# Performance work log

Hardware: AMD Instinct MI355X
Metric: run time of the kernel (lower is better)

## Reference

```python
import jax, jax.numpy as jnp
import numpy as np
import math

B, S, HID = 2, 2048, 2048
H, HKV, D, L = 16, 4, 128, 64
THETA = 10000.0
N_REP = H // HKV


def _rope(t, pos, theta=THETA):
    # t: [B, h, S, D], pos: [B, S] int
    d = t.shape[-1]
    inv_freq = 1.0 / (theta ** (jnp.arange(0, d, 2, dtype=jnp.float32) / d))  # [d/2]
    ang = pos.astype(jnp.float32)[:, :, None] * inv_freq  # [B, S, d/2]
    cos = jnp.concatenate([jnp.cos(ang), jnp.cos(ang)], axis=-1)[:, None]  # [B,1,S,d]
    sin = jnp.concatenate([jnp.sin(ang), jnp.sin(ang)], axis=-1)[:, None]
    t1, t2 = t[..., : d // 2], t[..., d // 2 :]
    rot = jnp.concatenate([-t2, t1], axis=-1)
    return t * cos + rot * sin


def setup_inputs() -> dict:
    key = jax.random.key(0)
    ks = jax.random.split(key, 9)
    sc = lambda fin: 1.0 / math.sqrt(fin)
    x = jax.random.normal(ks[0], (B, S, HID), dtype=jnp.float32)
    position_ids = jnp.broadcast_to(jnp.arange(S, dtype=jnp.int32), (B, S))
    # additive causal mask [1,1,S,S]
    causal = jnp.triu(jnp.full((S, S), -1e9, dtype=jnp.float32), k=1)
    attention_mask = causal[None, None]
    Wq = jax.random.normal(ks[1], (HID, H * D), dtype=jnp.float32) * sc(HID)
    Wk = jax.random.normal(ks[2], (HID, HKV * D), dtype=jnp.float32) * sc(HID)
    Wv = jax.random.normal(ks[3], (HID, HKV * D), dtype=jnp.float32) * sc(HID)
    Wql = jax.random.normal(ks[4], (D, L), dtype=jnp.float32) * sc(D)
    Wkl = jax.random.normal(ks[5], (D, L), dtype=jnp.float32) * sc(D)
    Wvl = jax.random.normal(ks[6], (D, L), dtype=jnp.float32) * sc(D)
    Wo = jax.random.normal(ks[7], (H * D, HID), dtype=jnp.float32) * sc(H * D)
    return {"x": x, "position_ids": position_ids, "attention_mask": attention_mask,
            "Wq": Wq, "Wk": Wk, "Wv": Wv, "Wql": Wql, "Wkl": Wkl, "Wvl": Wvl, "Wo": Wo}


def reference(x, position_ids, attention_mask, Wq, Wk, Wv, Wql, Wkl, Wvl, Wo):
    b, s, _ = x.shape
    q = (x @ Wq).reshape(b, s, H, D).transpose(0, 2, 1, 3)    # [B,H,S,D]
    k = (x @ Wk).reshape(b, s, HKV, D).transpose(0, 2, 1, 3)  # [B,HKV,S,D]
    v = (x @ Wv).reshape(b, s, HKV, D).transpose(0, 2, 1, 3)
    q = _rope(q, position_ids)
    k = _rope(k, position_ids)
    # latent compression per head-dim
    q_l = jnp.einsum('bhsd,dl->bhsl', q, Wql)  # [B,H,S,L]
    k_l = jnp.einsum('bhsd,dl->bhsl', k, Wkl)  # [B,HKV,S,L]
    v_l = jnp.einsum('bhsd,dl->bhsl', v, Wvl)
    k_l = jnp.repeat(k_l, N_REP, axis=1)  # repeat_kv -> [B,H,S,L]
    v_l = jnp.repeat(v_l, N_REP, axis=1)
    scale = math.sqrt(L)
    attn = jnp.einsum('bhql,bhkl->bhqk', q_l, k_l) / scale
    attn = attn + attention_mask
    attn = jax.nn.softmax(attn, axis=-1)
    out = jnp.einsum('bhqk,bhkl->bhql', attn, v_l)  # [B,H,S,L]
    if L < D:
        out = jnp.pad(out, ((0, 0), (0, 0), (0, 0), (0, D - L)))
    out = out.transpose(0, 2, 1, 3).reshape(b, s, H * D)
    return out @ Wo
```

## Files before the change

kernel.cpp:

```cpp
#include <hip/hip_runtime.h>
#include <cstddef>

constexpr int kB   = 2;
constexpr int kS   = 2048;
constexpr int kHID = 2048;
constexpr int kH   = 16;
constexpr int kHKV = 4;
constexpr int kD   = 128;
constexpr int kL   = 64;
constexpr int kTok = kB * kS;
constexpr int kNQKV = kH * kD + 2 * kHKV * kD;

typedef __attribute__((ext_vector_type(8))) short bf16x8;
typedef __attribute__((ext_vector_type(4))) float f32x4;

static __device__ __forceinline__ short f2bf(float f) {
  union { float f; unsigned u; } v{f};
  const unsigned r = (v.u + 0x7fff + ((v.u >> 16) & 1)) >> 16;
  return (short)r;
}
static __device__ __forceinline__ float bf2f(short s) {
  union { unsigned u; float f; } v;
  v.u = ((unsigned)(unsigned short)s) << 16;
  return v.f;
}

static __device__ __forceinline__ bf16x8 pack8(float4 a, float4 b) {
  bf16x8 r;
  r[0] = f2bf(a.x); r[1] = f2bf(a.y); r[2] = f2bf(a.z); r[3] = f2bf(a.w);
  r[4] = f2bf(b.x); r[5] = f2bf(b.y); r[6] = f2bf(b.z); r[7] = f2bf(b.w);
  return r;
}

static __device__ __forceinline__ unsigned cvt_pk_bf16(float lo, float hi) {
  unsigned r;
  asm("v_cvt_pk_bf16_f32 %0, %1, %2" : "=v"(r) : "v"(lo), "v"(hi));
  return r;
}

typedef __attribute__((address_space(3))) void       lds_void;
typedef __attribute__((address_space(1))) const void gm_void;
static __device__ __forceinline__ void gload16(const void* g, void* l) {
  __builtin_amdgcn_global_load_lds((gm_void*)g, (lds_void*)l, 16, 0, 0);
}

static __device__ __forceinline__ int2 xcd_swz(int nx, int ny) {
  int wg = blockIdx.y * nx + blockIdx.x;
  const int cpx = (nx * ny) >> 3;
  wg = (wg & 7) * cpx + (wg >> 3);
  int2 r; r.x = wg % nx; r.y = wg / nx;
  return r;
}

__global__ __launch_bounds__(256) void cvt_bf16(const float* __restrict__ in,
                                                short* __restrict__ out, int n8) {
  const int i = blockIdx.x * 256 + threadIdx.x;
  if (i >= n8) return;
  const float4 a = *(const float4*)&in[i * 8];
  const float4 b = *(const float4*)&in[i * 8 + 4];
  *(bf16x8*)&out[i * 8] = pack8(a, b);
}

__global__ __launch_bounds__(256) void trig_table(const int* __restrict__ pos,
                                                  float* __restrict__ tbl) {
  const int idx = blockIdx.x * 256 + threadIdx.x;
  if (idx >= kTok * 64) return;
  const int i = idx & 63, t = idx >> 6;
  const float p = (float)pos[t];
  const float inv_freq = expf(-(float)i * (9.210340371976184f / 64.0f));
  const float ang = p * inv_freq;
  tbl[t * 128 + i]      = cosf(ang);
  tbl[t * 128 + 64 + i] = sinf(ang);
}

template <bool REMAP>
__global__ __launch_bounds__(256) void transpose_cvt(
    const float* __restrict__ in, short* __restrict__ out,
    int Nin, int out_ld, int row_off, float scale) {
  __shared__ float T[64][65];
  const int tid = threadIdx.x;
  const int k0 = blockIdx.y * 64, n0 = blockIdx.x * 64;
  const int rr = tid >> 4;
  const int cc = tid & 15;
#pragma unroll
  for (int ii = 0; ii < 4; ++ii) {
    const int kr = rr + ii * 16;
    int gr = k0 + kr;
    if (REMAP) gr = ((gr >> 6) << 7) + (gr & 63);
    const float4 v = *(const float4*)&in[(size_t)gr * Nin + n0 + cc * 4];
    T[kr][cc * 4 + 0] = v.x * scale; T[kr][cc * 4 + 1] = v.y * scale;
    T[kr][cc * 4 + 2] = v.z * scale; T[kr][cc * 4 + 3] = v.w * scale;
  }
  __syncthreads();
#pragma unroll
  for (int ii = 0; ii < 4; ++ii) {
    const int n = rr + ii * 16;
    const short4 s4 = make_short4(f2bf(T[cc * 4 + 0][n]), f2bf(T[cc * 4 + 1][n]),
                                  f2bf(T[cc * 4 + 2][n]), f2bf(T[cc * 4 + 3][n]));
    *(short4*)&out[(size_t)(row_off + n0 + n) * out_ld + k0 + cc * 4] = s4;
  }
}

__global__ __launch_bounds__(256) void transpose_lat3(
    const float* __restrict__ Wql, const float* __restrict__ Wkl,
    const float* __restrict__ Wvl, short* __restrict__ WqlT,
    short* __restrict__ WklT, short* __restrict__ WvlT) {
  __shared__ float T[64][65];
  const float* in; short* out; float scale;
  if (blockIdx.z == 0)      { in = Wql; out = WqlT; scale = 0.125f; }
  else if (blockIdx.z == 1) { in = Wkl; out = WklT; scale = 1.0f; }
  else                      { in = Wvl; out = WvlT; scale = 1.0f; }
  const int tid = threadIdx.x;
  const int k0 = blockIdx.y * 64;
  const int rr = tid >> 4, cc = tid & 15;
#pragma unroll
  for (int ii = 0; ii < 4; ++ii) {
    const int kr = rr + ii * 16;
    const float4 v = *(const float4*)&in[(size_t)(k0 + kr) * kL + cc * 4];
    T[kr][cc * 4 + 0] = v.x * scale; T[kr][cc * 4 + 1] = v.y * scale;
    T[kr][cc * 4 + 2] = v.z * scale; T[kr][cc * 4 + 3] = v.w * scale;
  }
  __syncthreads();
#pragma unroll
  for (int ii = 0; ii < 4; ++ii) {
    const int n = rr + ii * 16;
    const short4 s4 = make_short4(f2bf(T[cc * 4 + 0][n]), f2bf(T[cc * 4 + 1][n]),
                                  f2bf(T[cc * 4 + 2][n]), f2bf(T[cc * 4 + 3][n]));
    *(short4*)&out[(size_t)n * kD + k0 + cc * 4] = s4;
  }
}

__global__ __launch_bounds__(512) void gemm_qkv8(
    const short* __restrict__ A, const short* __restrict__ Bt,
    short* __restrict__ C0, short* __restrict__ C1, short* __restrict__ C2,
    int K) {
  __shared__ short As[2][256 * 64];
  __shared__ short Bs[2][256 * 64];
  const int tid = threadIdx.x;
  const int lane = tid & 63, w = tid >> 6;
  const int lr = lane & 15, lk = lane >> 4;
  const int wm = w >> 2, wn = w & 3;
  const int2 sw = xcd_swz(kNQKV / 256, kTok / 256);
  const int row0 = sw.y * 256, col0 = sw.x * 256;
  const int NT = K >> 6;

  auto stage = [&](int kt) {
    const int b = kt & 1;
    const int k0 = kt << 6;
#pragma unroll
    for (int j = 0; j < 4; ++j) {
      const int idx = j * 512 + tid;
      const int row = idx >> 3, blk = idx & 7;
      const int gcol = k0 + ((blk ^ (row & 7)) << 3);
      gload16(A + (size_t)(row0 + row) * K + gcol, &As[b][row * 64 + blk * 8]);
    }
#pragma unroll
    for (int j = 0; j < 4; ++j) {
      const int idx = j * 512 + tid;
      const int row = idx >> 3, blk = idx & 7;
      const int gcol = k0 + ((blk ^ (row & 7)) << 3);
      gload16(Bt + (size_t)(col0 + row) * K + gcol, &Bs[b][row * 64 + blk * 8]);
    }
  };

  f32x4 acc[8][4] = {};

  stage(0);
  for (int t = 0; t < NT; ++t) {
    const int b = t & 1;
    if (t + 1 < NT) {
      stage(t + 1);
      asm volatile("s_waitcnt vmcnt(8)" ::: "memory");
    } else {
      asm volatile("s_waitcnt vmcnt(0)" ::: "memory");
    }
    __builtin_amdgcn_s_barrier();

    bf16x8 bb[4][2];
#pragma unroll
    for (int n = 0; n < 4; ++n) {
      const int row = wn * 64 + n * 16 + lr;
#pragma unroll
      for (int ch = 0; ch < 2; ++ch) {
        const int blk = (ch * 4 + lk) ^ (row & 7);
        bb[n][ch] = *(const bf16x8*)&Bs[b][row * 64 + blk * 8];
      }
    }
#pragma unroll
    for (int qm = 0; qm < 2; ++qm) {
      bf16x8 a[4][2];
#pragma unroll
      for (int j = 0; j < 4; ++j) {
        const int row = wm * 128 + (qm * 4 + j) * 16 + lr;
#pragma unroll
        for (int ch = 0; ch < 2; ++ch) {
          const int blk = (ch * 4 + lk) ^ (row & 7);
          a[j][ch] = *(const bf16x8*)&As[b][row * 64 + blk * 8];
        }
      }
      __builtin_amdgcn_s_setprio(1);
#pragma unroll
      for (int j = 0; j < 4; ++j)
#pragma unroll
        for (int n = 0; n < 4; ++n)
#pragma unroll
          for (int ch = 0; ch < 2; ++ch)
            acc[qm * 4 + j][n] = __builtin_amdgcn_mfma_f32_16x16x32_bf16(
                a[j][ch], bb[n][ch], acc[qm * 4 + j][n], 0, 0, 0);
      __builtin_amdgcn_s_setprio(0);
    }
    __builtin_amdgcn_s_barrier();
  }

  short* dst; int ld, cb;
  if (col0 < 2048)      { dst = C0; ld = 2048; cb = col0; }
  else if (col0 < 2560) { dst = C1; ld = 512;  cb = col0 - 2048; }
  else                  { dst = C2; ld = 512;  cb = col0 - 2560; }
  const int crow0 = row0 + wm * 128 + lk * 4;
  const int ccol0 = cb + wn * 64 + lr;
#pragma unroll
  for (int mf = 0; mf < 8; ++mf)
#pragma unroll
    for (int nf = 0; nf < 4; ++nf)
#pragma unroll
      for (int r = 0; r < 4; ++r)
        dst[(size_t)(crow0 + mf * 16 + r) * ld + ccol0 + nf * 16] =
            f2bf(acc[mf][nf][r]);
}

__global__ __launch_bounds__(256) void gemm_mfma(
    const short* __restrict__ A, const short* __restrict__ Bt,
    float* __restrict__ C0, int M, int N, int K) {
  __shared__ short As[128 * 32];
  __shared__ short Bs[128 * 32];
  const int tid = threadIdx.x;
  const int l = tid & 63, w = tid >> 6;
  const int lr = l & 15, lk = l >> 4;
  const int wm = w >> 1, wn = w & 1;
  const int2 sw = xcd_swz(N / 128, M / 128);
  const int row0 = sw.y * 128, col0 = sw.x * 128;

  f32x4 acc[4][4] = {};

  for (int k0 = 0; k0 < K; k0 += 32) {
    __syncthreads();
#pragma unroll
    for (int j = 0; j < 2; ++j) {
      const int idx = j * 256 + tid;
      const int r = idx >> 2, c = idx & 3;
      gload16(A  + (size_t)(row0 + r) * K + k0 + c * 8, &As[idx * 8]);
      gload16(Bt + (size_t)(col0 + r) * K + k0 + c * 8, &Bs[idx * 8]);
    }
    __syncthreads();
    bf16x8 af[4], bfr[4];
#pragma unroll
    for (int m = 0; m < 4; ++m)
      af[m] = *(const bf16x8*)&As[(wm * 64 + m * 16 + lr) * 32 + lk * 8];
#pragma unroll
    for (int n = 0; n < 4; ++n)
      bfr[n] = *(const bf16x8*)&Bs[(wn * 64 + n * 16 + lr) * 32 + lk * 8];
#pragma unroll
    for (int m = 0; m < 4; ++m)
#pragma unroll
      for (int n = 0; n < 4; ++n)
        acc[m][n] = __builtin_amdgcn_mfma_f32_16x16x32_bf16(af[m], bfr[n],
                                                            acc[m][n], 0, 0, 0);
  }

  const int crow0 = row0 + wm * 64 + lk * 4;
  const int ccol0 = col0 + wn * 64 + lr;
#pragma unroll
  for (int m = 0; m < 4; ++m)
#pragma unroll
    for (int n = 0; n < 4; ++n)
#pragma unroll
      for (int rr = 0; rr < 4; ++rr)
        C0[(size_t)(crow0 + m * 16 + rr) * N + ccol0 + n * 16] = acc[m][n][rr];
}

__global__ __launch_bounds__(256) void rope_latent_all(
    const short* __restrict__ qb, const short* __restrict__ kb,
    const short* __restrict__ vb, const short* __restrict__ WqlT,
    const short* __restrict__ WklT, const short* __restrict__ WvlT,
    const float* __restrict__ tbl, short* __restrict__ q_l,
    short* __restrict__ k_l, short* __restrict__ v_lT) {
  __shared__ short Tw[4][1280];
  const int yz = blockIdx.y;
  const short* in; const short* WT; short* out; int nh; bool ROPE, TR;
  int bh;
  if (yz < 32)      { in = qb; WT = WqlT; out = q_l;  nh = kH;   ROPE = true;  TR = false; bh = yz; }
  else if (yz < 40) { in = kb; WT = WklT; out = k_l;  nh = kHKV; ROPE = true;  TR = false; bh = yz - 32; }
  else              { in = vb; WT = WvlT; out = v_lT; nh = kHKV; ROPE = false; TR = true;  bh = yz - 40; }

  const int tid = threadIdx.x;
  const int lane = tid & 63;
  const int w = tid >> 6;
  const int lr = lane & 15;
  const int lk = lane >> 4;
  const int b = bh / nh, h = bh % nh;
  const int s0 = blockIdx.x * 64;
  const int srow = s0 + w * 16 + lr;
  const int tok = b * kS + srow;

  const short* ip = in + ((size_t)tok * nh + h) * kD + lk * 8;
  bf16x8 raw[4];
#pragma unroll
  for (int ch = 0; ch < 4; ++ch) raw[ch] = *(const bf16x8*)(ip + ch * 32);

  bf16x8 af[4];
  if (ROPE) {
    float a[4][8];
#pragma unroll
    for (int ch = 0; ch < 4; ++ch)
#pragma unroll
      for (int i = 0; i < 8; ++i) a[ch][i] = bf2f(raw[ch][i]);
    const float* tb = tbl + (size_t)tok * 128;
    float c[2][8], sn[2][8];
#pragma unroll
    for (int g = 0; g < 2; ++g) {
      const float4 cA = *(const float4*)(tb + g * 32 + lk * 8);
      const float4 cB = *(const float4*)(tb + g * 32 + lk * 8 + 4);
      const float4 sA = *(const float4*)(tb + 64 + g * 32 + lk * 8);
      const float4 sB = *(const float4*)(tb + 64 + g * 32 + lk * 8 + 4);
      c[g][0] = cA.x; c[g][1] = cA.y; c[g][2] = cA.z; c[g][3] = cA.w;
      c[g][4] = cB.x; c[g][5] = cB.y; c[g][6] = cB.z; c[g][7] = cB.w;
      sn[g][0] = sA.x; sn[g][1] = sA.y; sn[g][2] = sA.z; sn[g][3] = sA.w;
      sn[g][4] = sB.x; sn[g][5] = sB.y; sn[g][6] = sB.z; sn[g][7] = sB.w;
    }
    float o[4][8];
#pragma unroll
    for (int g = 0; g < 2; ++g)
#pragma unroll
      for (int i = 0; i < 8; ++i) {
        o[g][i]     = a[g][i]     * c[g][i] - a[g + 2][i] * sn[g][i];
        o[g + 2][i] = a[g + 2][i] * c[g][i] + a[g][i]     * sn[g][i];
      }
#pragma unroll
    for (int ch = 0; ch < 4; ++ch)
#pragma unroll
      for (int i = 0; i < 8; ++i) af[ch][i] = f2bf(o[ch][i]);
  } else {
#pragma unroll
    for (int ch = 0; ch < 4; ++ch) af[ch] = raw[ch];
  }

  f32x4 acc[4] = {};
#pragma unroll
  for (int cb = 0; cb < 4; ++cb) {
#pragma unroll
    for (int ch = 0; ch < 4; ++ch) {
      const bf16x8 bfrag =
          *(const bf16x8*)&WT[(size_t)(cb * 16 + lr) * kD + ch * 32 + lk * 8];
      acc[cb] = __builtin_amdgcn_mfma_f32_16x16x32_bf16(af[ch], bfrag,
                                                        acc[cb], 0, 0, 0);
    }
  }

  short* T = Tw[w];
  if (!TR) {
#pragma unroll
    for (int cb = 0; cb < 4; ++cb)
#pragma unroll
      for (int r = 0; r < 4; ++r)
        T[(lk * 4 + r) * 72 + cb * 16 + lr] = f2bf(acc[cb][r]);
    asm volatile("s_waitcnt lgkmcnt(0)" ::: "memory");
#pragma unroll
    for (int it = 0; it < 2; ++it) {
      const int idx = it * 64 + lane;
      const int row = idx >> 3, c8 = (idx & 7) << 3;
      *(bf16x8*)&out[((size_t)bh * kS + s0 + w * 16 + row) * kL + c8] =
          *(const bf16x8*)&T[row * 72 + c8];
    }
  } else {
#pragma unroll
    for (int cb = 0; cb < 4; ++cb)
#pragma unroll
      for (int r = 0; r < 4; ++r)
        T[(cb * 16 + lr) * 20 + lk * 4 + r] = f2bf(acc[cb][r]);
    asm volatile("s_waitcnt lgkmcnt(0)" ::: "memory");
    const size_t orow = ((size_t)bh * kL + lane) * kS + s0 + w * 16;
#pragma unroll
    for (int c = 0; c < 4; ++c)
      *(short4*)&out[orow + c * 4] = *(const short4*)&T[lane * 20 + c * 4];
  }
}

__global__ __launch_bounds__(512) void flash_attn_mfma(
    const short* __restrict__ ql, const short* __restrict__ kl,
    const short* __restrict__ vlT, short* __restrict__ attn_out) {
  constexpr int LDK = 72;
  __shared__ short Kt[2][64 * LDK];
  __shared__ short Vt[2][64 * LDK];
  __shared__ short Pt[128 * LDK];

  const int tid = threadIdx.x;
  const int lane = tid & 63;
  const int w = tid >> 6;
  const int lr = lane & 15;
  const int lk = lane >> 4;
  const int bid = blockIdx.y;
  const int bx = (bid < 8) ? (2 * bid) : (31 - 2 * bid);
  const int q0 = bx * 128;
  const int bh = blockIdx.x;
  const int b = bh >> 4, h = bh & 15;
  const int hk = h >> 2;
  const int wrow = q0 + w * 16;

  const short* qrow = ql + ((size_t)bh * kS + wrow + lr) * kL;
  bf16x8 qf[2];
  qf[0] = *(const bf16x8*)(qrow + lk * 8);
  qf[1] = *(const bf16x8*)(qrow + 32 + lk * 8);

  f32x4 Of[4] = {};
  float m_r[4], l_r[4];
#pragma unroll
  for (int r = 0; r < 4; ++r) { m_r[r] = -3.0e38f; l_r[r] = 0.f; }

  const size_t kbase = (size_t)(b * kHKV + hk) * kS * kL;
  const size_t vbase = (size_t)(b * kHKV + hk) * kL * kS;
  const int ntiles = q0 / 64 + 2;
  const int sr = tid >> 3, sc8 = (tid & 7) << 3;
  const short* kp = kl + kbase + (size_t)sr * kL + sc8;
  const short* vp = vlT + vbase + (size_t)sr * kS + sc8;

  *(bf16x8*)&Kt[0][sr * LDK + sc8] = *(const bf16x8*)kp;
  *(bf16x8*)&Vt[0][sr * LDK + sc8] = *(const bf16x8*)vp;
  __syncthreads();

  int cur = 0;
  for (int t = 0; t < ntiles; ++t) {
    const int j0 = t * 64;
    const bool pre = (t + 1 < ntiles);
    bf16x8 krn, vrn;
    if (pre) {
      krn = *(const bf16x8*)(kp + (size_t)(j0 + 64) * kL);
      vrn = *(const bf16x8*)(vp + (j0 + 64));
    }

    if (j0 <= wrow) {
      const short* Kc = &Kt[cur][0];
      const short* Vc = &Vt[cur][0];

      f32x4 Sf[4];
      __builtin_amdgcn_s_setprio(1);
#pragma unroll
      for (int cb = 0; cb < 4; ++cb) {
        f32x4 acc = {};
#pragma unroll
        for (int ch = 0; ch < 2; ++ch) {
          const bf16x8 kf = *(const bf16x8*)&Kc[(cb * 16 + lr) * LDK + ch * 32 + lk * 8];
          acc = __builtin_amdgcn_mfma_f32_16x16x32_bf16(qf[ch], kf, acc, 0, 0, 0);
        }
        Sf[cb] = acc;
      }
      __builtin_amdgcn_s_setprio(0);

      const bool diag = (j0 + 63 > wrow);
      float mt[4] = {-3.0e38f, -3.0e38f, -3.0e38f, -3.0e38f};
#pragma unroll
      for (int cb = 0; cb < 4; ++cb)
#pragma unroll
        for (int r = 0; r < 4; ++r) {
          float s = Sf[cb][r];
          if (diag && (j0 + cb * 16 + lr) > (wrow + lk * 4 + r)) s = -3.0e38f;
          Sf[cb][r] = s;
          mt[r] = fmaxf(mt[r], s);
        }
#pragma unroll
      for (int d = 1; d < 16; d <<= 1)
#pragma unroll
        for (int r = 0; r < 4; ++r) mt[r] = fmaxf(mt[r], __shfl_xor(mt[r], d));

      const bool need = (mt[0] > m_r[0] + 8.f) || (mt[1] > m_r[1] + 8.f) ||
                        (mt[2] > m_r[2] + 8.f) || (mt[3] > m_r[3] + 8.f);
      const bool resc = __any((int)need);
      float corr[4] = {1.f, 1.f, 1.f, 1.f};
      if (resc) {
#pragma unroll
        for (int r = 0; r < 4; ++r) {
          const float mnew = fmaxf(m_r[r], mt[r]);
          corr[r] = __expf(m_r[r] - mnew);
          m_r[r] = mnew;
          l_r[r] *= corr[r];
        }
      }
#pragma unroll
      for (int cb = 0; cb < 4; ++cb) {
        const float p0 = __expf(Sf[cb][0] - m_r[0]);
        const float p1 = __expf(Sf[cb][1] - m_r[1]);
        const float p2 = __expf(Sf[cb][2] - m_r[2]);
        const float p3 = __expf(Sf[cb][3] - m_r[3]);
        l_r[0] += p0; l_r[1] += p1; l_r[2] += p2; l_r[3] += p3;
        const unsigned pk01 = cvt_pk_bf16(p0, p1);
        const unsigned pk23 = cvt_pk_bf16(p2, p3);
        short* prow = &Pt[(w * 16 + lk * 4) * LDK + cb * 16 + lr];
        prow[0 * LDK] = (short)(pk01 & 0xffff);
        prow[1 * LDK] = (short)(pk01 >> 16);
        prow[2 * LDK] = (short)(pk23 & 0xffff);
        prow[3 * LDK] = (short)(pk23 >> 16);
      }
      asm volatile("s_waitcnt lgkmcnt(0)" ::: "memory");

      __builtin_amdgcn_s_setprio(1);
#pragma unroll
      for (int cb = 0; cb < 4; ++cb) {
        f32x4 acc = Of[cb];
        if (resc) {
#pragma unroll
          for (int r = 0; r < 4; ++r) acc[r] *= corr[r];
        }
#pragma unroll
        for (int ch = 0; ch < 2; ++ch) {
          const bf16x8 pf = *(const bf16x8*)&Pt[(w * 16 + lr) * LDK + ch * 32 + lk * 8];
          const bf16x8 vf = *(const bf16x8*)&Vc[(cb * 16 + lr) * LDK + ch * 32 + lk * 8];
          acc = __builtin_amdgcn_mfma_f32_16x16x32_bf16(pf, vf, acc, 0, 0, 0);
        }
        Of[cb] = acc;
      }
      __builtin_amdgcn_s_setprio(0);
    }

    if (pre) {
      *(bf16x8*)&Kt[cur ^ 1][sr * LDK + sc8] = krn;
      *(bf16x8*)&Vt[cur ^ 1][sr * LDK + sc8] = vrn;
    }
    __syncthreads();
    cur ^= 1;
  }

#pragma unroll
  for (int d = 1; d < 16; d <<= 1)
#pragma unroll
    for (int r = 0; r < 4; ++r) l_r[r] += __shfl_xor(l_r[r], d);

#pragma unroll
  for (int r = 0; r < 4; ++r) {
    const float inv = 1.f / l_r[r];
    const size_t row = (size_t)(b * kS + wrow + lk * 4 + r) * (kH * kL);
#pragma unroll
    for (int cb = 0; cb < 4; ++cb)
      attn_out[row + h * kL + cb * 16 + lr] = f2bf(Of[cb][r] * inv);
  }
}

extern "C" void kernel_launch(void* const* d_in, const int* in_sizes, int n_in,
                              void* d_out, int out_size, void* d_ws, size_t ws_size,
                              hipStream_t stream) {
  const float* x    = (const float*)d_in[0];
  const int*   pos  = (const int*)d_in[1];
  const float* Wq   = (const float*)d_in[3];
  const float* Wk   = (const float*)d_in[4];
  const float* Wv   = (const float*)d_in[5];
  const float* Wql  = (const float*)d_in[6];
  const float* Wkl  = (const float*)d_in[7];
  const float* Wvl  = (const float*)d_in[8];
  const float* Wo   = (const float*)d_in[9];
  float* out = (float*)d_out;

  char* p = (char*)d_ws;
  short* x_bf  = (short*)p; p += (size_t)kTok * kHID * 2;
  short* Wqkv  = (short*)p; p += (size_t)kNQKV * kHID * 2;
  short* WoT   = (short*)p; p += (size_t)kHID * (kH * kL) * 2;
  short* WqlT  = (short*)p; p += (size_t)kL * kD * 2;
  short* WklT  = (short*)p; p += (size_t)kL * kD * 2;
  short* WvlT  = (short*)p; p += (size_t)kL * kD * 2;
  float* tbl   = (float*)p; p += (size_t)kTok * 128 * 4;
  short* k_buf = (short*)p; p += (size_t)kTok * kHKV * kD * 2;
  short* v_buf = (short*)p; p += (size_t)kTok * kHKV * kD * 2;
  short* q_l   = (short*)p; p += (size_t)kB * kH * kS * kL * 2;
  short* k_l   = (short*)p; p += (size_t)kB * kHKV * kS * kL * 2;
  short* v_lT  = (short*)p; p += (size_t)kB * kHKV * kS * kL * 2;
  short* attn  = (short*)p;
  short* q_buf = (short*)d_out;

  cvt_bf16<<<kTok * kHID / 8 / 256, 256, 0, stream>>>(x, x_bf, kTok * kHID / 8);
  trig_table<<<kTok * 64 / 256, 256, 0, stream>>>(pos, tbl);
  transpose_cvt<false><<<dim3(kH * kD / 64, kHID / 64), 256, 0, stream>>>(
      Wq, Wqkv, kH * kD, kHID, 0, 1.0f);
  transpose_cvt<false><<<dim3(kHKV * kD / 64, kHID / 64), 256, 0, stream>>>(
      Wk, Wqkv, kHKV * kD, kHID, kH * kD, 1.0f);
  transpose_cvt<false><<<dim3(kHKV * kD / 64, kHID / 64), 256, 0, stream>>>(
      Wv, Wqkv, kHKV * kD, kHID, kH * kD + kHKV * kD, 1.0f);
  transpose_cvt<true><<<dim3(kHID / 64, (kH * kL) / 64), 256, 0, stream>>>(
      Wo, WoT, kHID, kH * kL, 0, 1.0f);
  transpose_lat3<<<dim3(1, kD / 64, 3), 256, 0, stream>>>(
      Wql, Wkl, Wvl, WqlT, WklT, WvlT);

  gemm_qkv8<<<dim3(kNQKV / 256, kTok / 256), 512, 0, stream>>>(
      x_bf, Wqkv, q_buf, k_buf, v_buf, kHID);

  rope_latent_all<<<dim3(kS / 64, 48), 256, 0, stream>>>(
      q_buf, k_buf, v_buf, WqlT, WklT, WvlT, tbl, q_l, k_l, v_lT);

  flash_attn_mfma<<<dim3(kB * kH, kS / 128), 512, 0, stream>>>(
      q_l, k_l, v_lT, attn);

  gemm_mfma<<<dim3(kHID / 128, kTok / 128), 256, 0, stream>>>(
      attn, WoT, out, kTok, kHID, kH * kL);
}
```

Before: 211.7 us.

## Merge QKV weight transposes, rewrite output GEMM with double-buffered swizzled tiles

The three Wq/Wk/Wv transpose-convert launches become one kernel that picks its source matrix per block. The output projection GEMM is rewritten with 256x128 tiles, 512 threads, K-step 64, double-buffered XOR-swizzled LDS, and async prefetch overlapped with MFMA via vmcnt waits. The flash attention mask loop now skips the per-element causal check on off-diagonal tiles. The aim is to cut launch overhead, LDS bank conflicts and load stalls in the output GEMM. The cost is higher LDS and register use per block, which may lower occupancy.

```diff
diff --git a/kernel.cpp b/kernel.cpp
--- a/kernel.cpp
+++ b/kernel.cpp
@@ -71,6 +71,34 @@
   const float ang = p * inv_freq;
   tbl[t * 128 + i]      = cosf(ang);
   tbl[t * 128 + 64 + i] = sinf(ang);
+}
+
+__global__ __launch_bounds__(256) void transpose_qkv(
+    const float* __restrict__ Wq, const float* __restrict__ Wk,
+    const float* __restrict__ Wv, short* __restrict__ out) {
+  __shared__ float T[64][65];
+  const int n0 = blockIdx.x * 64, k0 = blockIdx.y * 64;
+  const float* in; int Nin, nl0;
+  if (n0 < 2048)      { in = Wq; Nin = 2048; nl0 = n0; }
+  else if (n0 < 2560) { in = Wk; Nin = 512;  nl0 = n0 - 2048; }
+  else                { in = Wv; Nin = 512;  nl0 = n0 - 2560; }
+  const int tid = threadIdx.x;
+  const int rr = tid >> 4, cc = tid & 15;
+#pragma unroll
+  for (int ii = 0; ii < 4; ++ii) {
+    const int kr = rr + ii * 16;
+    const float4 v = *(const float4*)&in[(size_t)(k0 + kr) * Nin + nl0 + cc * 4];
+    T[kr][cc * 4 + 0] = v.x; T[kr][cc * 4 + 1] = v.y;
+    T[kr][cc * 4 + 2] = v.z; T[kr][cc * 4 + 3] = v.w;
+  }
+  __syncthreads();
+#pragma unroll
+  for (int ii = 0; ii < 4; ++ii) {
+    const int n = rr + ii * 16;
+    const short4 s4 = make_short4(f2bf(T[cc * 4 + 0][n]), f2bf(T[cc * 4 + 1][n]),
+                                  f2bf(T[cc * 4 + 2][n]), f2bf(T[cc * 4 + 3][n]));
+    *(short4*)&out[(size_t)(n0 + n) * kHID + k0 + cc * 4] = s4;
+  }
 }
 
 template <bool REMAP>
@@ -228,54 +256,96 @@
             f2bf(acc[mf][nf][r]);
 }
 
-__global__ __launch_bounds__(256) void gemm_mfma(
+__global__ __launch_bounds__(512) void gemm_out8(
     const short* __restrict__ A, const short* __restrict__ Bt,
-    float* __restrict__ C0, int M, int N, int K) {
-  __shared__ short As[128 * 32];
-  __shared__ short Bs[128 * 32];
+    float* __restrict__ C, int M, int N, int K) {
+  __shared__ short As[2][256 * 64];
+  __shared__ short Bs[2][128 * 64];
   const int tid = threadIdx.x;
-  const int l = tid & 63, w = tid >> 6;
-  const int lr = l & 15, lk = l >> 4;
-  const int wm = w >> 1, wn = w & 1;
-  const int2 sw = xcd_swz(N / 128, M / 128);
-  const int row0 = sw.y * 128, col0 = sw.x * 128;
-
-  f32x4 acc[4][4] = {};
-
-  for (int k0 = 0; k0 < K; k0 += 32) {
-    __syncthreads();
+  const int lane = tid & 63, w = tid >> 6;
+  const int lr = lane & 15, lk = lane >> 4;
+  const int wm = w >> 2, wn = w & 3;
+  const int2 sw = xcd_swz(N / 128, M / 256);
+  const int row0 = sw.y * 256, col0 = sw.x * 128;
+  const int NT = K >> 6;
+
+  auto stage = [&](int kt) {
+    const int b = kt & 1;
+    const int k0 = kt << 6;
+#pragma unroll
+    for (int j = 0; j < 4; ++j) {
+      const int idx = j * 512 + tid;
+      const int row = idx >> 3, blk = idx & 7;
+      const int gcol = k0 + ((blk ^ (row & 7)) << 3);
+      gload16(A + (size_t)(row0 + row) * K + gcol, &As[b][row * 64 + blk * 8]);
+    }
 #pragma unroll
     for (int j = 0; j < 2; ++j) {
-      const int idx = j * 256 + tid;
-      const int r = idx >> 2, c = idx & 3;
-      gload16(A  + (size_t)(row0 + r) * K + k0 + c * 8, &As[idx * 8]);
-      gload16(Bt + (size_t)(col0 + r) * K + k0 + c * 8, &Bs[idx * 8]);
-    }
-    __syncthreads();
-    bf16x8 af[4], bfr[4];
-#pragma unroll
-    for (int m = 0; m < 4; ++m)
-      af[m] = *(const bf16x8*)&As[(wm * 64 + m * 16 + lr) * 32 + lk * 8];
-#pragma unroll
-    for (int n = 0; n < 4; ++n)
-      bfr[n] = *(const bf16x8*)&Bs[(wn * 64 + n * 16 + lr) * 32 + lk * 8];
-#pragma unroll
-    for (int m = 0; m < 4; ++m)
-#pragma unroll
-      for (int n = 0; n < 4; ++n)
-        acc[m][n] = __builtin_amdgcn_mfma_f32_16x16x32_bf16(af[m], bfr[n],
-                                                            acc[m][n], 0, 0, 0);
-  }
-
-  const int crow0 = row0 + wm * 64 + lk * 4;
-  const int ccol0 = col0 + wn * 64 + lr;
-#pragma unroll
-  for (int m = 0; m < 4; ++m)
-#pragma unroll
-    for (int n = 0; n < 4; ++n)
-#pragma unroll
-      for (int rr = 0; rr < 4; ++rr)
-        C0[(size_t)(crow0 + m * 16 + rr) * N + ccol0 + n * 16] = acc[m][n][rr];
+      const int idx = j * 512 + tid;
+      const int row = idx >> 3, blk = idx & 7;
+      const int gcol = k0 + ((blk ^ (row & 7)) << 3);
+      gload16(Bt + (size_t)(col0 + row) * K + gcol, &Bs[b][row * 64 + blk * 8]);
+    }
+  };
+
+  f32x4 acc[8][2] = {};
+
+  stage(0);
+  for (int t = 0; t < NT; ++t) {
+    const int b = t & 1;
+    if (t + 1 < NT) {
+      stage(t + 1);
+      asm volatile("s_waitcnt vmcnt(6)" ::: "memory");
+    } else {
+      asm volatile("s_waitcnt vmcnt(0)" ::: "memory");
+    }
+    __builtin_amdgcn_s_barrier();
+
+    bf16x8 bb[2][2];
+#pragma unroll
+    for (int n = 0; n < 2; ++n) {
+      const int row = wn * 32 + n * 16 + lr;
+#pragma unroll
+      for (int ch = 0; ch < 2; ++ch) {
+        const int blk = (ch * 4 + lk) ^ (row & 7);
+        bb[n][ch] = *(const bf16x8*)&Bs[b][row * 64 + blk * 8];
+      }
+    }
+#pragma unroll
+    for (int qm = 0; qm < 2; ++qm) {
+      bf16x8 a[4][2];
+#pragma unroll
+      for (int j = 0; j < 4; ++j) {
+        const int row = wm * 128 + (qm * 4 + j) * 16 + lr;
+#pragma unroll
+        for (int ch = 0; ch < 2; ++ch) {
+          const int blk = (ch * 4 + lk) ^ (row & 7);
+          a[j][ch] = *(const bf16x8*)&As[b][row * 64 + blk * 8];
+        }
+      }
+      __builtin_amdgcn_s_setprio(1);
+#pragma unroll
+      for (int j = 0; j < 4; ++j)
+#pragma unroll
+        for (int n = 0; n < 2; ++n)
+#pragma unroll
+          for (int ch = 0; ch < 2; ++ch)
+            acc[qm * 4 + j][n] = __builtin_amdgcn_mfma_f32_16x16x32_bf16(
+                a[j][ch], bb[n][ch], acc[qm * 4 + j][n], 0, 0, 0);
+      __builtin_amdgcn_s_setprio(0);
+    }
+    __builtin_amdgcn_s_barrier();
+  }
+
+  const int crow0 = row0 + wm * 128 + lk * 4;
+  const int ccol0 = col0 + wn * 32 + lr;
+#pragma unroll
+  for (int mf = 0; mf < 8; ++mf)
+#pragma unroll
+    for (int nf = 0; nf < 2; ++nf)
+#pragma unroll
+      for (int r = 0; r < 4; ++r)
+        C[(size_t)(crow0 + mf * 16 + r) * N + ccol0 + nf * 16] = acc[mf][nf][r];
 }
 
 __global__ __launch_bounds__(256) void rope_latent_all(
@@ -455,17 +525,23 @@
       }
       __builtin_amdgcn_s_setprio(0);
 
-      const bool diag = (j0 + 63 > wrow);
       float mt[4] = {-3.0e38f, -3.0e38f, -3.0e38f, -3.0e38f};
-#pragma unroll
-      for (int cb = 0; cb < 4; ++cb)
-#pragma unroll
-        for (int r = 0; r < 4; ++r) {
-          float s = Sf[cb][r];
-          if (diag && (j0 + cb * 16 + lr) > (wrow + lk * 4 + r)) s = -3.0e38f;
-          Sf[cb][r] = s;
-          mt[r] = fmaxf(mt[r], s);
-        }
+      if (j0 + 63 > wrow) {
+#pragma unroll
+        for (int cb = 0; cb < 4; ++cb)
+#pragma unroll
+          for (int r = 0; r < 4; ++r) {
+            float s = Sf[cb][r];
+            if ((j0 + cb * 16 + lr) > (wrow + lk * 4 + r)) s = -3.0e38f;
+            Sf[cb][r] = s;
+            mt[r] = fmaxf(mt[r], s);
+          }
+      } else {
+#pragma unroll
+        for (int cb = 0; cb < 4; ++cb)
+#pragma unroll
+          for (int r = 0; r < 4; ++r) mt[r] = fmaxf(mt[r], Sf[cb][r]);
+      }
 #pragma unroll
       for (int d = 1; d < 16; d <<= 1)
 #pragma unroll
@@ -575,12 +651,8 @@
 
   cvt_bf16<<<kTok * kHID / 8 / 256, 256, 0, stream>>>(x, x_bf, kTok * kHID / 8);
   trig_table<<<kTok * 64 / 256, 256, 0, stream>>>(pos, tbl);
-  transpose_cvt<false><<<dim3(kH * kD / 64, kHID / 64), 256, 0, stream>>>(
-      Wq, Wqkv, kH * kD, kHID, 0, 1.0f);
-  transpose_cvt<false><<<dim3(kHKV * kD / 64, kHID / 64), 256, 0, stream>>>(
-      Wk, Wqkv, kHKV * kD, kHID, kH * kD, 1.0f);
-  transpose_cvt<false><<<dim3(kHKV * kD / 64, kHID / 64), 256, 0, stream>>>(
-      Wv, Wqkv, kHKV * kD, kHID, kH * kD + kHKV * kD, 1.0f);
+  transpose_qkv<<<dim3(kNQKV / 64, kHID / 64), 256, 0, stream>>>(
+      Wq, Wk, Wv, Wqkv);
   transpose_cvt<true><<<dim3(kHID / 64, (kH * kL) / 64), 256, 0, stream>>>(
       Wo, WoT, kHID, kH * kL, 0, 1.0f);
   transpose_lat3<<<dim3(1, kD / 64, 3), 256, 0, stream>>>(
@@ -595,6 +667,6 @@
   flash_attn_mfma<<<dim3(kB * kH, kS / 128), 512, 0, stream>>>(
       q_l, k_l, v_lT, attn);
 
-  gemm_mfma<<<dim3(kHID / 128, kTok / 128), 256, 0, stream>>>(
+  gemm_out8<<<dim3(kHID / 128, kTok / 256), 512, 0, stream>>>(
       attn, WoT, out, kTok, kHID, kH * kL);
 }
```

After: 200.1 us. -5.5%, faster.
